# Kernel optimization log

Hardware: AMD Instinct MI355X
Metric: run time of the kernel (lower is better)

Reference implementation:

```python
import jax, jax.numpy as jnp
import numpy as np

B, V, NF, K = 16, 5000, 352, 120


def setup_inputs() -> dict:
    key = jax.random.key(0)
    k1, k2, k3, k4 = jax.random.split(key, 4)
    return {
        "feat_x": jax.random.normal(k1, (B, V, NF), dtype=jnp.float32),
        "feat_y": jax.random.normal(k2, (B, V, NF), dtype=jnp.float32),
        "evecs_x": jax.random.normal(k3, (B, V, K), dtype=jnp.float32),
        "evecs_y": jax.random.normal(k4, (B, V, K), dtype=jnp.float32),
    }


def reference(feat_x, feat_y, evecs_x, evecs_y):
    # Spectral coefficients: F_hat[b] = (evecs_x[b]^T feat_x[b])^T -> [B, F, K]
    F_hat = jnp.einsum("bvk,bvf->bfk", evecs_x, feat_x)
    G_hat = jnp.einsum("bvk,bvf->bfk", evecs_y, feat_y)

    # C1[b] = (inv(F^T F) F^T G)^T, batched least-squares solve
    FtF = jnp.einsum("bfk,bfl->bkl", F_hat, F_hat)  # [B,K,K]
    FtG = jnp.einsum("bfk,bfl->bkl", F_hat, G_hat)  # [B,K,K]
    C1 = jnp.linalg.solve(FtF, FtG).transpose(0, 2, 1)

    GtG = jnp.einsum("bfk,bfl->bkl", G_hat, G_hat)
    GtF = jnp.einsum("bfk,bfl->bkl", G_hat, F_hat)
    C2 = jnp.linalg.solve(GtG, GtF).transpose(0, 2, 1)
    return (C1, C2)
```

## Files before the change

kernel.cpp:

```cpp
#include <hip/hip_runtime.h>
#include <hip/hip_bf16.h>

#define NB 16
#define VV 5000
#define NFD 352
#define KD 120
#define NCH 5
#define SLABSZ (352 * 120)

typedef __attribute__((ext_vector_type(8))) short short8;
typedef __attribute__((ext_vector_type(4))) float float4v;

__device__ __forceinline__ void load_lds16(const float* g, float* l) {
    __builtin_amdgcn_global_load_lds(
        (const __attribute__((address_space(1))) unsigned int*)g,
        (__attribute__((address_space(3))) unsigned int*)l, 16, 0, 0);
}

__device__ __forceinline__ unsigned short bfb(float a) {
    return __builtin_bit_cast(unsigned short, __float2bfloat16(a));
}

__device__ __forceinline__ void pack8(const float* f, int4& hi, int4& lo) {
    unsigned short h[8], l[8];
    #pragma unroll
    for (int j = 0; j < 8; ++j) {
        const float a = f[j];
        const __hip_bfloat16 hb = __float2bfloat16(a);
        h[j] = __builtin_bit_cast(unsigned short, hb);
        l[j] = bfb(a - __bfloat162float(hb));
    }
    hi.x = h[0] | (h[1] << 16); hi.y = h[2] | (h[3] << 16);
    hi.z = h[4] | (h[5] << 16); hi.w = h[6] | (h[7] << 16);
    lo.x = l[0] | (l[1] << 16); lo.y = l[2] | (l[3] << 16);
    lo.z = l[4] | (l[5] << 16); lo.w = l[6] | (l[7] << 16);
}

template <int RS>
__device__ __forceinline__ void frag_from_lds(const float* base, int col, int g,
                                              short8& hi8, short8& lo8) {
    float f[8];
    #pragma unroll
    for (int j = 0; j < 8; ++j) {
        const int v = g * 8 + j;
        f[j] = base[v * RS + (((col >> 2) ^ (v & 7)) << 2) + (col & 3)];
    }
    int4 hi, lo;
    pack8(f, hi, lo);
    hi8 = __builtin_bit_cast(short8, hi);
    lo8 = __builtin_bit_cast(short8, lo);
}

__global__ __launch_bounds__(256, 4) void proj_mfma(
    const float* __restrict__ fx, const float* __restrict__ fy,
    const float* __restrict__ ex, const float* __restrict__ ey,
    float* __restrict__ partials, const float* __restrict__ zeropad)
{
    const int t = threadIdx.x;

    int lin = blockIdx.x + 30 * (blockIdx.y + 2 * blockIdx.z);
    lin = (lin & 7) * 120 + (lin >> 3);
    const int xx   = lin % 30;
    const int rest = lin / 30;
    const int wh = rest & 1;
    const int b  = rest >> 1;
    const int mt = xx % 6;
    const int ch = xx / 6;

    const float* Ab = (wh ? fy : fx) + (size_t)b * VV * NFD;
    const float* Bb = (wh ? ey : ex) + (size_t)b * VV * KD;
    const int m0 = mt * 64;

    __shared__ float lds[6144];

    const float* aSrc[2]; int av[2];
    #pragma unroll
    for (int i = 0; i < 2; ++i) {
        const int u = i * 256 + t;
        const int v = u >> 4;
        const int gg = u & 15;
        const int lg = gg ^ (v & 7);
        const int col = min(m0 + lg * 4, NFD - 4);
        aSrc[i] = Ab + col;
        av[i] = v;
    }
    const float* bSrc[4]; int bv[4]; bool bok[4];
    #pragma unroll
    for (int i = 0; i < 4; ++i) {
        const int u = i * 256 + t;
        const int v = u >> 5;
        const int gg = u & 31;
        const int lg = gg ^ (v & 7);
        const int col = lg * 4;
        bok[i] = (col < KD);
        bSrc[i] = Bb + (bok[i] ? col : 0);
        bv[i] = v;
    }

    const int lane = t & 63;
    const int wid  = t >> 6;
    const int wm = wid >> 1, wn = wid & 1;
    const int r16 = lane & 15;
    const int g   = lane >> 4;

    float4v acc[2][4];
    #pragma unroll
    for (int mf = 0; mf < 2; ++mf)
        #pragma unroll
        for (int nf = 0; nf < 4; ++nf)
            acc[mf][nf] = float4v{0.f, 0.f, 0.f, 0.f};

    const int chv0 = ch * 1024;
    const int nst  = (ch < 4) ? 32 : 29;

    for (int st = 0; st < nst; ++st) {
        const int v0 = chv0 + st * 32;

        #pragma unroll
        for (int i = 0; i < 2; ++i) {
            const int vg = v0 + av[i];
            const float* src = (vg < VV) ? (aSrc[i] + (size_t)vg * NFD) : zeropad;
            load_lds16(src, &lds[(i * 256 + t) * 4]);
        }
        #pragma unroll
        for (int i = 0; i < 4; ++i) {
            const int vg = v0 + bv[i];
            const float* src = (bok[i] && vg < VV) ? (bSrc[i] + (size_t)vg * KD) : zeropad;
            load_lds16(src, &lds[2048 + (i * 256 + t) * 4]);
        }
        __syncthreads();

        short8 bh[4], bl[4];
        #pragma unroll
        for (int nf = 0; nf < 4; ++nf)
            frag_from_lds<128>(&lds[2048], wn * 64 + nf * 16 + r16, g, bh[nf], bl[nf]);

        #pragma unroll
        for (int mf = 0; mf < 2; ++mf) {
            short8 ah, al;
            frag_from_lds<64>(&lds[0], wm * 32 + mf * 16 + r16, g, ah, al);
            #pragma unroll
            for (int nf = 0; nf < 4; ++nf) {
                acc[mf][nf] = __builtin_amdgcn_mfma_f32_16x16x32_bf16(ah, bh[nf], acc[mf][nf], 0, 0, 0);
                acc[mf][nf] = __builtin_amdgcn_mfma_f32_16x16x32_bf16(ah, bl[nf], acc[mf][nf], 0, 0, 0);
                acc[mf][nf] = __builtin_amdgcn_mfma_f32_16x16x32_bf16(al, bh[nf], acc[mf][nf], 0, 0, 0);
            }
        }
        __syncthreads();
    }

    float* slab = partials + (size_t)((ch * 2 + wh) * NB + b) * SLABSZ;
    #pragma unroll
    for (int mf = 0; mf < 2; ++mf) {
        const int mrow = mt * 64 + wm * 32 + mf * 16 + g * 4;
        #pragma unroll
        for (int nf = 0; nf < 4; ++nf) {
            const int n = wn * 64 + nf * 16 + r16;
            if (n < KD) {
                #pragma unroll
                for (int r = 0; r < 4; ++r) {
                    const int m = mrow + r;
                    if (m < NFD) slab[(size_t)m * KD + n] = acc[mf][nf][r];
                }
            }
        }
    }
}

__global__ __launch_bounds__(256) void reduce_k(
    const float* __restrict__ partials, float* __restrict__ fhat, float* __restrict__ ghat)
{
    const int id = blockIdx.x * 256 + threadIdx.x;
    if (id >= NFD * KD) return;
    const int wb = blockIdx.y;
    const int wh = wb >> 4;
    const int b  = wb & 15;

    const float* p = partials + (size_t)(wh * NB + b) * SLABSZ + id;
    const size_t chstride = (size_t)2 * NB * SLABSZ;

    float s = 0.f;
    #pragma unroll
    for (int c = 0; c < NCH; ++c) s += p[c * chstride];

    float* dst = (wh ? ghat : fhat) + (size_t)b * NFD * KD + id;
    *dst = s;
}

__device__ __forceinline__ void gemm_tn_64x64(
    const float* __restrict__ A, const float* __restrict__ B, float* __restrict__ C,
    int V, int M, int N, int m0, int n0)
{
    __shared__ float As[16][64];
    __shared__ float Bs[16][64];

    const int tid = threadIdx.x;
    const int tx = tid & 15;
    const int ty = tid >> 4;
    const int sr = tid >> 4;
    const int sc = (tid & 15) << 2;

    float acc[4][4] = {{0.f,0.f,0.f,0.f},{0.f,0.f,0.f,0.f},
                       {0.f,0.f,0.f,0.f},{0.f,0.f,0.f,0.f}};

    for (int v0 = 0; v0 < V; v0 += 16) {
        const int v = v0 + sr;
        float4 av; av.x = av.y = av.z = av.w = 0.f;
        float4 bv; bv.x = bv.y = bv.z = bv.w = 0.f;
        if (v < V) {
            const float* Ar = A + (size_t)v * M;
            const int ca = m0 + sc;
            if (ca + 3 < M) {
                av = *(const float4*)(Ar + ca);
            } else {
                if (ca + 0 < M) av.x = Ar[ca + 0];
                if (ca + 1 < M) av.y = Ar[ca + 1];
                if (ca + 2 < M) av.z = Ar[ca + 2];
                if (ca + 3 < M) av.w = Ar[ca + 3];
            }
            const float* Br = B + (size_t)v * N;
            const int cb = n0 + sc;
            if (cb + 3 < N) {
                bv = *(const float4*)(Br + cb);
            } else {
                if (cb + 0 < N) bv.x = Br[cb + 0];
                if (cb + 1 < N) bv.y = Br[cb + 1];
                if (cb + 2 < N) bv.z = Br[cb + 2];
                if (cb + 3 < N) bv.w = Br[cb + 3];
            }
        }
        __syncthreads();
        *(float4*)&As[sr][sc] = av;
        *(float4*)&Bs[sr][sc] = bv;
        __syncthreads();

        #pragma unroll
        for (int kk = 0; kk < 16; ++kk) {
            const float4 a4 = *(const float4*)&As[kk][ty << 2];
            const float4 b4 = *(const float4*)&Bs[kk][tx << 2];
            const float a[4]  = {a4.x, a4.y, a4.z, a4.w};
            const float bb[4] = {b4.x, b4.y, b4.z, b4.w};
            #pragma unroll
            for (int i = 0; i < 4; ++i)
                #pragma unroll
                for (int j = 0; j < 4; ++j)
                    acc[i][j] = fmaf(a[i], bb[j], acc[i][j]);
        }
    }

    #pragma unroll
    for (int i = 0; i < 4; ++i) {
        const int m = m0 + (ty << 2) + i;
        if (m < M) {
            #pragma unroll
            for (int j = 0; j < 4; ++j) {
                const int n = n0 + (tx << 2) + j;
                if (n < N) C[(size_t)m * N + n] = acc[i][j];
            }
        }
    }
}

__global__ __launch_bounds__(256) void gram_kernel(
    const float* __restrict__ fhat, const float* __restrict__ ghat,
    float* __restrict__ ftf, float* __restrict__ gtg, float* __restrict__ ftg)
{
    const int b = blockIdx.z;
    const int which = blockIdx.y;
    const int m0 = (blockIdx.x & 1) * 64;
    const int n0 = (blockIdx.x >> 1) * 64;

    const float* F = fhat + (size_t)b * NFD * KD;
    const float* G = ghat + (size_t)b * NFD * KD;
    const float* A  = (which == 1) ? G : F;
    const float* Bp = (which == 0) ? F : G;
    float* C = ((which == 0) ? ftf : (which == 1) ? gtg : ftg) + (size_t)b * KD * KD;

    gemm_tn_64x64(A, Bp, C, NFD, KD, KD, m0, n0);
}

__device__ __forceinline__ float ldval(const float* __restrict__ A, const float* __restrict__ B,
                                       int pair, int row, int col) {
    if (col < KD) return A[row * KD + col];
    const int l = col - KD;
    return pair ? B[l * KD + row] : B[row * KD + l];
}

#define FOR15(OP) OP(0) OP(1) OP(2) OP(3) OP(4) OP(5) OP(6) OP(7) OP(8) OP(9) \
                  OP(10) OP(11) OP(12) OP(13) OP(14)

__global__ __launch_bounds__(480, 1) void solve_kernel(
    const float* __restrict__ ftf, const float* __restrict__ gtg,
    const float* __restrict__ ftg, float* __restrict__ out)
{
    const int pair = blockIdx.x;
    const int b = blockIdx.y;
    const int tid = threadIdx.x;
    const int cg = tid & 15;
    const int rg = tid >> 4;
    const int cbase = cg * 15;
    const int r0 = rg * 4;
    const int seg = cg * 20;

    const float* Ag = ((pair == 0) ? ftf : gtg) + (size_t)b * KD * KD;
    const float* Bg = ftg + (size_t)b * KD * KD;

    __shared__ __align__(16) float prow[2][320];
    __shared__ __align__(16) float pcol[2][120];

    #define DECL(I) float w##I = ldval(Ag, Bg, pair, r0 + 0, cbase + (I)); \
                    float x##I = ldval(Ag, Bg, pair, r0 + 1, cbase + (I)); \
                    float y##I = ldval(Ag, Bg, pair, r0 + 2, cbase + (I)); \
                    float z##I = ldval(Ag, Bg, pair, r0 + 3, cbase + (I));
    FOR15(DECL)
    #undef DECL

    if (rg == 0) {
        #define PUB0(I) prow[0][seg + (I)] = w##I;
        FOR15(PUB0)
        #undef PUB0
    }
    if (cg == 0) *(float4*)&pcol[0][r0] = float4{w0, x0, y0, z0};
    __syncthreads();

    int jseg = 0, joff = 0;

    for (int j = 0; j < KD; ++j) {
        const int cur = j & 1;
        const int nxt = cur ^ 1;

        const float pinv = 1.0f / prow[cur][jseg * 20 + joff];
        const float4 f4 = *(const float4*)&pcol[cur][r0];

        const float4 q0 = *(const float4*)&prow[cur][seg + 0];
        const float4 q1 = *(const float4*)&prow[cur][seg + 4];
        const float4 q2 = *(const float4*)&prow[cur][seg + 8];
        const float4 q3 = *(const float4*)&prow[cur][seg + 12];
        const float p0 = q0.x, p1 = q0.y, p2 = q0.z, p3 = q0.w;
        const float p4 = q1.x, p5 = q1.y, p6 = q1.z, p7 = q1.w;
        const float p8 = q2.x, p9 = q2.y, p10 = q2.z, p11 = q2.w;
        const float p12 = q3.x, p13 = q3.y, p14 = q3.z;

        const float fw = f4.x * pinv, fx = f4.y * pinv;
        const float fy = f4.z * pinv, fz = f4.w * pinv;

        #define UPD(I) w##I = fmaf(-fw, p##I, w##I); x##I = fmaf(-fx, p##I, x##I); \
                       y##I = fmaf(-fy, p##I, y##I); z##I = fmaf(-fz, p##I, z##I);
        FOR15(UPD)
        #undef UPD

        if (rg == (j >> 2)) {
            #define FW(I) w##I = p##I * pinv;
            #define FX(I) x##I = p##I * pinv;
            #define FY(I) y##I = p##I * pinv;
            #define FZ(I) z##I = p##I * pinv;
            switch (j & 3) {
                case 0: FOR15(FW) break;
                case 1: FOR15(FX) break;
                case 2: FOR15(FY) break;
                default: FOR15(FZ) break;
            }
            #undef FW
            #undef FX
            #undef FY
            #undef FZ
        }

        const int j2 = j + 1;

        if (j2 < KD && rg == (j2 >> 2)) {
            #define PW(I) prow[nxt][seg + (I)] = w##I;
            #define PX(I) prow[nxt][seg + (I)] = x##I;
            #define PY(I) prow[nxt][seg + (I)] = y##I;
            #define PZ(I) prow[nxt][seg + (I)] = z##I;
            switch (j2 & 3) {
                case 0: FOR15(PW) break;
                case 1: FOR15(PX) break;
                case 2: FOR15(PY) break;
                default: FOR15(PZ) break;
            }
            #undef PW
            #undef PX
            #undef PY
            #undef PZ
        }

        joff++; if (joff == 15) { joff = 0; jseg++; }
        if (j2 < KD && cg == jseg) {
            #define PC(I) case I: *(float4*)&pcol[nxt][r0] = float4{w##I, x##I, y##I, z##I}; break;
            switch (joff) {
                FOR15(PC)
                default: break;
            }
            #undef PC
        }
        __syncthreads();
    }

    if (cg >= 8) {
        float* op = out + (size_t)pair * NB * KD * KD + (size_t)b * KD * KD;
        #define OUTW(I) { const int l = cbase + (I) - KD; \
                          *(float4*)&op[l * KD + r0] = float4{w##I, x##I, y##I, z##I}; }
        FOR15(OUTW)
        #undef OUTW
    }
}

extern "C" void kernel_launch(void* const* d_in, const int* in_sizes, int n_in,
                              void* d_out, int out_size, void* d_ws, size_t ws_size,
                              hipStream_t stream)
{
    const float* feat_x  = (const float*)d_in[0];
    const float* feat_y  = (const float*)d_in[1];
    const float* evecs_x = (const float*)d_in[2];
    const float* evecs_y = (const float*)d_in[3];
    float* out = (float*)d_out;

    float* ws       = (float*)d_ws;
    float* zeropad  = ws;
    float* partials = ws + 64;
    float* fhat     = partials + (size_t)NCH * 2 * NB * SLABSZ;
    float* ghat     = fhat + (size_t)NB * NFD * KD;
    float* ftf      = ws + 64;
    float* gtg      = ftf + (size_t)NB * KD * KD;
    float* ftg      = gtg + (size_t)NB * KD * KD;

    hipMemsetAsync(zeropad, 0, 256, stream);

    proj_mfma <<<dim3(30, 2, NB), 256, 0, stream>>>(feat_x, feat_y, evecs_x, evecs_y, partials, zeropad);
    reduce_k  <<<dim3(165, 32), 256, 0, stream>>>(partials, fhat, ghat);
    gram_kernel<<<dim3(4, 3, NB), 256, 0, stream>>>(fhat, ghat, ftf, gtg, ftg);
    solve_kernel<<<dim3(2, NB), 480, 0, stream>>>(ftf, gtg, ftg, out);
}
```

Measured before the change: 247.4 us.

## Prefetch projection tiles into registers and store pre-split bf16 fragments in LDS

The projection kernel stops using async global-to-LDS copies of fp32 tiles. Each thread now loads the next k-step into registers with scalar strided loads while MFMAs run on the current tile. It then splits the values into bf16 hi/lo once and writes them to LDS in MFMA-fragment layout, so fragments are read with single 16-byte loads and no per-wave repacking. This removes redundant conversion work and the zeropad buffer and memset, but uses scalar uncoalesced-style global loads, more registers and a larger LDS footprint (30 KB), which may reduce occupancy.

```diff
diff --git a/kernel.cpp b/kernel.cpp
--- a/kernel.cpp
+++ b/kernel.cpp
@@ -11,12 +11,6 @@
 typedef __attribute__((ext_vector_type(8))) short short8;
 typedef __attribute__((ext_vector_type(4))) float float4v;
 
-__device__ __forceinline__ void load_lds16(const float* g, float* l) {
-    __builtin_amdgcn_global_load_lds(
-        (const __attribute__((address_space(1))) unsigned int*)g,
-        (__attribute__((address_space(3))) unsigned int*)l, 16, 0, 0);
-}
-
 __device__ __forceinline__ unsigned short bfb(float a) {
     return __builtin_bit_cast(unsigned short, __float2bfloat16(a));
 }
@@ -36,25 +30,10 @@
     lo.z = l[4] | (l[5] << 16); lo.w = l[6] | (l[7] << 16);
 }
 
-template <int RS>
-__device__ __forceinline__ void frag_from_lds(const float* base, int col, int g,
-                                              short8& hi8, short8& lo8) {
-    float f[8];
-    #pragma unroll
-    for (int j = 0; j < 8; ++j) {
-        const int v = g * 8 + j;
-        f[j] = base[v * RS + (((col >> 2) ^ (v & 7)) << 2) + (col & 3)];
-    }
-    int4 hi, lo;
-    pack8(f, hi, lo);
-    hi8 = __builtin_bit_cast(short8, hi);
-    lo8 = __builtin_bit_cast(short8, lo);
-}
-
 __global__ __launch_bounds__(256, 4) void proj_mfma(
     const float* __restrict__ fx, const float* __restrict__ fy,
     const float* __restrict__ ex, const float* __restrict__ ey,
-    float* __restrict__ partials, const float* __restrict__ zeropad)
+    float* __restrict__ partials)
 {
     const int t = threadIdx.x;
 
@@ -71,31 +50,18 @@
     const float* Bb = (wh ? ey : ex) + (size_t)b * VV * KD;
     const int m0 = mt * 64;
 
-    __shared__ float lds[6144];
-
-    const float* aSrc[2]; int av[2];
-    #pragma unroll
-    for (int i = 0; i < 2; ++i) {
-        const int u = i * 256 + t;
-        const int v = u >> 4;
-        const int gg = u & 15;
-        const int lg = gg ^ (v & 7);
-        const int col = min(m0 + lg * 4, NFD - 4);
-        aSrc[i] = Ab + col;
-        av[i] = v;
-    }
-    const float* bSrc[4]; int bv[4]; bool bok[4];
-    #pragma unroll
-    for (int i = 0; i < 4; ++i) {
-        const int u = i * 256 + t;
-        const int v = u >> 5;
-        const int gg = u & 31;
-        const int lg = gg ^ (v & 7);
-        const int col = lg * 4;
-        bok[i] = (col < KD);
-        bSrc[i] = Bb + (bok[i] ? col : 0);
-        bv[i] = v;
-    }
+    __shared__ __align__(16) unsigned char lds[30720];
+
+    const int am = t & 63;
+    const int ao = t >> 6;
+    const float* aSrc = Ab + min(m0 + am, NFD - 1);
+    const int awb = am * 80 + ao * 16;
+    const int bn0 = t & 127;
+    const int bo0 = (t >> 7) & 3;
+    const int bo1 = ((256 + t) >> 7) & 3;
+    const float* bSrc0 = Bb + min(bn0, KD - 1);
+    const int bwb0 = bn0 * 80 + bo0 * 16;
+    const int bwb1 = bn0 * 80 + bo1 * 16;
 
     const int lane = t & 63;
     const int wid  = t >> 6;
@@ -103,6 +69,14 @@
     const int r16 = lane & 15;
     const int g   = lane >> 4;
 
+    int aoffs[2], boffs[4];
+    #pragma unroll
+    for (int mf = 0; mf < 2; ++mf)
+        aoffs[mf] = (wm * 32 + mf * 16 + r16) * 80 + g * 16;
+    #pragma unroll
+    for (int nf = 0; nf < 4; ++nf)
+        boffs[nf] = 10240 + (wn * 64 + nf * 16 + r16) * 80 + g * 16;
+
     float4v acc[2][4];
     #pragma unroll
     for (int mf = 0; mf < 2; ++mf)
@@ -113,40 +87,87 @@
     const int chv0 = ch * 1024;
     const int nst  = (ch < 4) ? 32 : 29;
 
-    for (int st = 0; st < nst; ++st) {
+    float a8[8], b8a[8], b8b[8];
+
+    auto load_regs = [&](int st) {
         const int v0 = chv0 + st * 32;
-
-        #pragma unroll
-        for (int i = 0; i < 2; ++i) {
-            const int vg = v0 + av[i];
-            const float* src = (vg < VV) ? (aSrc[i] + (size_t)vg * NFD) : zeropad;
-            load_lds16(src, &lds[(i * 256 + t) * 4]);
-        }
-        #pragma unroll
-        for (int i = 0; i < 4; ++i) {
-            const int vg = v0 + bv[i];
-            const float* src = (bok[i] && vg < VV) ? (bSrc[i] + (size_t)vg * KD) : zeropad;
-            load_lds16(src, &lds[2048 + (i * 256 + t) * 4]);
-        }
-        __syncthreads();
-
-        short8 bh[4], bl[4];
-        #pragma unroll
-        for (int nf = 0; nf < 4; ++nf)
-            frag_from_lds<128>(&lds[2048], wn * 64 + nf * 16 + r16, g, bh[nf], bl[nf]);
-
+        const int va  = v0 + ao * 8;
+        const int vb0 = v0 + bo0 * 8;
+        const int vb1 = v0 + bo1 * 8;
+        if (v0 + 32 <= VV) {
+            #pragma unroll
+            for (int j = 0; j < 8; ++j) a8[j]  = aSrc [(size_t)(va  + j) * NFD];
+            #pragma unroll
+            for (int j = 0; j < 8; ++j) b8a[j] = bSrc0[(size_t)(vb0 + j) * KD];
+            #pragma unroll
+            for (int j = 0; j < 8; ++j) b8b[j] = bSrc0[(size_t)(vb1 + j) * KD];
+        } else {
+            #pragma unroll
+            for (int j = 0; j < 8; ++j) {
+                float v = 0.f;
+                if (va + j < VV) v = aSrc[(size_t)(va + j) * NFD];
+                a8[j] = v;
+            }
+            #pragma unroll
+            for (int j = 0; j < 8; ++j) {
+                float v = 0.f;
+                if (vb0 + j < VV) v = bSrc0[(size_t)(vb0 + j) * KD];
+                b8a[j] = v;
+            }
+            #pragma unroll
+            for (int j = 0; j < 8; ++j) {
+                float v = 0.f;
+                if (vb1 + j < VV) v = bSrc0[(size_t)(vb1 + j) * KD];
+                b8b[j] = v;
+            }
+        }
+    };
+
+    auto pack_write = [&]() {
+        int4 hi, lo;
+        pack8(a8, hi, lo);
+        *(int4*)(lds + awb)          = hi;
+        *(int4*)(lds + 5120 + awb)   = lo;
+        pack8(b8a, hi, lo);
+        *(int4*)(lds + 10240 + bwb0) = hi;
+        *(int4*)(lds + 20480 + bwb0) = lo;
+        pack8(b8b, hi, lo);
+        *(int4*)(lds + 10240 + bwb1) = hi;
+        *(int4*)(lds + 20480 + bwb1) = lo;
+    };
+
+    auto frag_mfma = [&]() {
+        short8 ah[2], al[2];
         #pragma unroll
         for (int mf = 0; mf < 2; ++mf) {
-            short8 ah, al;
-            frag_from_lds<64>(&lds[0], wm * 32 + mf * 16 + r16, g, ah, al);
-            #pragma unroll
-            for (int nf = 0; nf < 4; ++nf) {
-                acc[mf][nf] = __builtin_amdgcn_mfma_f32_16x16x32_bf16(ah, bh[nf], acc[mf][nf], 0, 0, 0);
-                acc[mf][nf] = __builtin_amdgcn_mfma_f32_16x16x32_bf16(ah, bl[nf], acc[mf][nf], 0, 0, 0);
-                acc[mf][nf] = __builtin_amdgcn_mfma_f32_16x16x32_bf16(al, bh[nf], acc[mf][nf], 0, 0, 0);
-            }
-        }
+            ah[mf] = *(const short8*)(lds + aoffs[mf]);
+            al[mf] = *(const short8*)(lds + 5120 + aoffs[mf]);
+        }
+        #pragma unroll
+        for (int nf = 0; nf < 4; ++nf) {
+            const short8 bh = *(const short8*)(lds + boffs[nf]);
+            const short8 bl = *(const short8*)(lds + 10240 + boffs[nf]);
+            #pragma unroll
+            for (int mf = 0; mf < 2; ++mf) {
+                acc[mf][nf] = __builtin_amdgcn_mfma_f32_16x16x32_bf16(ah[mf], bh, acc[mf][nf], 0, 0, 0);
+                acc[mf][nf] = __builtin_amdgcn_mfma_f32_16x16x32_bf16(ah[mf], bl, acc[mf][nf], 0, 0, 0);
+                acc[mf][nf] = __builtin_amdgcn_mfma_f32_16x16x32_bf16(al[mf], bh, acc[mf][nf], 0, 0, 0);
+            }
+        }
+    };
+
+    load_regs(0);
+    pack_write();
+    __syncthreads();
+
+    for (int st = 0; st < nst; ++st) {
+        if (st + 1 < nst) load_regs(st + 1);
+        frag_mfma();
         __syncthreads();
+        if (st + 1 < nst) {
+            pack_write();
+            __syncthreads();
+        }
     }
 
     float* slab = partials + (size_t)((ch * 2 + wh) * NB + b) * SLABSZ;
@@ -417,7 +438,6 @@
     float* out = (float*)d_out;
 
     float* ws       = (float*)d_ws;
-    float* zeropad  = ws;
     float* partials = ws + 64;
     float* fhat     = partials + (size_t)NCH * 2 * NB * SLABSZ;
     float* ghat     = fhat + (size_t)NB * NFD * KD;
@@ -425,9 +445,7 @@
     float* gtg      = ftf + (size_t)NB * KD * KD;
     float* ftg      = gtg + (size_t)NB * KD * KD;
 
-    hipMemsetAsync(zeropad, 0, 256, stream);
-
-    proj_mfma <<<dim3(30, 2, NB), 256, 0, stream>>>(feat_x, feat_y, evecs_x, evecs_y, partials, zeropad);
+    proj_mfma <<<dim3(30, 2, NB), 256, 0, stream>>>(feat_x, feat_y, evecs_x, evecs_y, partials);
     reduce_k  <<<dim3(165, 32), 256, 0, stream>>>(partials, fhat, ghat);
     gram_kernel<<<dim3(4, 3, NB), 256, 0, stream>>>(fhat, ghat, ftf, gtg, ftg);
     solve_kernel<<<dim3(2, NB), 480, 0, stream>>>(ftf, gtg, ftg, out);
```

Measured after the change: 218.6 us. 11.6% less time.
